# Kernel tuning notes

Hardware: AMD Instinct MI355X
Metric: run time of the kernel (lower is better)

## Reference

```python
import jax, jax.numpy as jnp
import numpy as np

B, S, D = 1, 2048, 4096
H, KVH, HD = 32, 8, 128


def setup_inputs() -> dict:
    key = jax.random.key(0)
    ks = jax.random.split(key, 6)
    x = jax.random.normal(ks[0], (B, S, D), dtype=jnp.float32)
    # Llama3 RoPE angles: theta = 500000
    inv_freq = 1.0 / (500000.0 ** (np.arange(0, HD, 2, dtype=np.float32) / HD))
    ang = np.arange(S, dtype=np.float32)[:, None] * inv_freq[None, :]  # [S, HD//2]
    freqs_cos = jnp.asarray(np.cos(ang), dtype=jnp.float32)
    freqs_sin = jnp.asarray(np.sin(ang), dtype=jnp.float32)
    sc = 0.02
    wq = jax.random.normal(ks[1], (H * HD, D), dtype=jnp.float32) * sc
    wk = jax.random.normal(ks[2], (KVH * HD, D), dtype=jnp.float32) * sc
    wv = jax.random.normal(ks[3], (KVH * HD, D), dtype=jnp.float32) * sc
    wo = jax.random.normal(ks[4], (D, H * HD), dtype=jnp.float32) * sc
    return {"x": x, "freqs_cos": freqs_cos, "freqs_sin": freqs_sin,
            "wq": wq, "wk": wk, "wv": wv, "wo": wo}


def _rope(t, cos, sin):
    # t: [B, S, h, HD]; rotate consecutive pairs (complex multiply)
    t2 = t.reshape(*t.shape[:-1], HD // 2, 2)
    x0, x1 = t2[..., 0], t2[..., 1]
    c = cos[None, :, None, :]
    s = sin[None, :, None, :]
    r0 = x0 * c - x1 * s
    r1 = x0 * s + x1 * c
    return jnp.stack([r0, r1], axis=-1).reshape(t.shape)


def reference(x, freqs_cos, freqs_sin, wq, wk, wv, wo):
    b, s, _ = x.shape
    q = jnp.einsum('bsd,ed->bse', x, wq).reshape(b, s, H, HD)
    k = jnp.einsum('bsd,ed->bse', x, wk).reshape(b, s, KVH, HD)
    v = jnp.einsum('bsd,ed->bse', x, wv).reshape(b, s, KVH, HD)
    q = _rope(q, freqs_cos, freqs_sin)
    k = _rope(k, freqs_cos, freqs_sin)
    # GQA: repeat kv heads
    rep = H // KVH
    k = jnp.repeat(k, rep, axis=2)
    v = jnp.repeat(v, rep, axis=2)
    scale = 1.0 / jnp.sqrt(jnp.asarray(HD, dtype=x.dtype))
    scores = jnp.einsum('bqhd,bkhd->bhqk', q, k) * scale
    causal = jnp.tril(jnp.ones((s, s), dtype=bool))
    scores = jnp.where(causal[None, None], scores, jnp.finfo(scores.dtype).min)
    p = jax.nn.softmax(scores, axis=-1)
    out = jnp.einsum('bhqk,bkhd->bqhd', p, v).reshape(b, s, H * HD)
    return jnp.einsum('bse,de->bsd', out, wo)
```

## Files before the change

kernel.cpp:

```cpp
#include <hip/hip_runtime.h>

typedef unsigned short u16;
typedef short bf16x8 __attribute__((ext_vector_type(8)));
typedef float f32x4 __attribute__((ext_vector_type(4)));

#define S_LEN 2048
#define ATT_SCALE (0.08838834764831845f * 1.4426950408889634f)
#define NEG_BIG  -1.0e30f

static __device__ __forceinline__ float bf2f(u16 u) {
  union { unsigned int i; float f; } v; v.i = ((unsigned int)u) << 16; return v.f;
}
static __device__ __forceinline__ u16 f2bf(float f) {
  union { float f; unsigned int i; } v; v.f = f;
  unsigned int x = v.i;
  return (u16)((x + 0x7fffu + ((x >> 16) & 1u)) >> 16);
}
static __device__ __forceinline__ float fexp2(float x) {
  return __builtin_amdgcn_exp2f(x);
}

static __device__ __forceinline__ void gl_lds16(const u16* g, u16* l) {
  __builtin_amdgcn_global_load_lds(
      (const __attribute__((address_space(1))) unsigned int*)g,
      (__attribute__((address_space(3))) unsigned int*)l, 16, 0, 0);
}

static __device__ __forceinline__ bf16x8 load8(const u16* p) { return *(const bf16x8*)p; }
static __device__ __forceinline__ bf16x8 load8(const float* p) {
  f32x4 a = *(const f32x4*)p;
  f32x4 b = *(const f32x4*)(p + 4);
  bf16x8 r;
  r[0] = (short)f2bf(a[0]); r[1] = (short)f2bf(a[1]);
  r[2] = (short)f2bf(a[2]); r[3] = (short)f2bf(a[3]);
  r[4] = (short)f2bf(b[0]); r[5] = (short)f2bf(b[1]);
  r[6] = (short)f2bf(b[2]); r[7] = (short)f2bf(b[3]);
  return r;
}
static __device__ __forceinline__ void store_out(u16* C, size_t i, float v)  { C[i] = f2bf(v); }
static __device__ __forceinline__ void store_out(float* C, size_t i, float v){ C[i] = v; }

__global__ __launch_bounds__(256) void f2b_kernel(
    const float* __restrict__ s, u16* __restrict__ d, int n8) {
  int i = blockIdx.x * 256 + threadIdx.x;
  if (i >= n8) return;
  *(bf16x8*)&d[(size_t)i * 8] = load8(s + (size_t)i * 8);
}

template <typename OT>
static __device__ __forceinline__ void gemm_core(
    const u16* __restrict__ A, const u16* __restrict__ B, OT* __restrict__ C,
    int K, int ldc, int bm, int bn) {
  __shared__ __align__(16) u16 As[128 * 64];
  __shared__ __align__(16) u16 Bs[128 * 64];
  const int tid  = threadIdx.x;
  const int lane = tid & 63;
  const int wave = tid >> 6;
  const int wm = (wave >> 1) << 6;
  const int wn = (wave & 1) << 6;
  const int col  = lane & 15;
  const int quad = lane >> 4;

  const f32x4 fzero = {0.f, 0.f, 0.f, 0.f};
  f32x4 acc[4][4];
#pragma unroll
  for (int i = 0; i < 4; ++i)
#pragma unroll
    for (int j = 0; j < 4; ++j) acc[i][j] = fzero;

  const int srow = (lane >> 3);
  const int sc8  = lane & 7;

  for (int k0 = 0; k0 < K; k0 += 64) {
#pragma unroll
    for (int i = 0; i < 4; ++i) {
      int r = wave * 32 + i * 8 + srow;
      int src = (sc8 ^ (r & 7)) << 3;
      gl_lds16(A + (size_t)(bm + r) * K + k0 + src, &As[(wave * 32 + i * 8) * 64]);
      gl_lds16(B + (size_t)(bn + r) * K + k0 + src, &Bs[(wave * 32 + i * 8) * 64]);
    }
    __syncthreads();
#pragma unroll
    for (int kk = 0; kk < 64; kk += 32) {
      bf16x8 af[4], bfr[4];
#pragma unroll
      for (int mt = 0; mt < 4; ++mt) {
        int row = wm + mt * 16 + col;
        af[mt] = *(const bf16x8*)&As[row * 64 + ((((kk >> 3) + quad) ^ (col & 7)) << 3)];
      }
#pragma unroll
      for (int nt = 0; nt < 4; ++nt) {
        int row = wn + nt * 16 + col;
        bfr[nt] = *(const bf16x8*)&Bs[row * 64 + ((((kk >> 3) + quad) ^ (col & 7)) << 3)];
      }
#pragma unroll
      for (int mt = 0; mt < 4; ++mt)
#pragma unroll
        for (int nt = 0; nt < 4; ++nt)
          acc[mt][nt] = __builtin_amdgcn_mfma_f32_16x16x32_bf16(
              af[mt], bfr[nt], acc[mt][nt], 0, 0, 0);
    }
    __syncthreads();
  }
#pragma unroll
  for (int mt = 0; mt < 4; ++mt)
#pragma unroll
    for (int nt = 0; nt < 4; ++nt)
#pragma unroll
      for (int r = 0; r < 4; ++r) {
        int row = bm + wm + mt * 16 + quad * 4 + r;
        int cn  = bn + wn + nt * 16 + col;
        store_out(C, (size_t)row * ldc + cn, acc[mt][nt][r]);
      }
}

__global__ __launch_bounds__(256) void gemm_qkv(
    const u16* __restrict__ xb, const u16* __restrict__ wqb,
    const u16* __restrict__ wkb, const u16* __restrict__ wvb,
    u16* __restrict__ q, u16* __restrict__ k, u16* __restrict__ v) {
  int bx = blockIdx.x;
  const u16* B; u16* C; int ldc, bn;
  if (bx < 32)      { B = wqb; C = q; ldc = 4096; bn = bx * 128; }
  else if (bx < 40) { B = wkb; C = k; ldc = 1024; bn = (bx - 32) * 128; }
  else              { B = wvb; C = v; ldc = 1024; bn = (bx - 40) * 128; }
  gemm_core<u16>(xb, B, C, 4096, ldc, blockIdx.y * 128, bn);
}

__global__ __launch_bounds__(256) void gemm_o(
    const u16* __restrict__ ao, const u16* __restrict__ wob, float* __restrict__ out) {
  gemm_core<float>(ao, wob, out, 4096, 4096, blockIdx.y * 128, blockIdx.x * 128);
}

#define LDK 72
template <typename AT, typename BT, typename OT>
__global__ __launch_bounds__(256) void gemm_bt(
    const AT* __restrict__ A, const BT* __restrict__ B,
    OT* __restrict__ C, int M, int N, int K) {
  __shared__ __align__(16) u16 As[128 * LDK];
  __shared__ __align__(16) u16 Bs[128 * LDK];
  const int tid  = threadIdx.x;
  const int lane = tid & 63;
  const int wave = tid >> 6;
  const int wm = (wave >> 1) << 6;
  const int wn = (wave & 1) << 6;
  const int col  = lane & 15;
  const int quad = lane >> 4;
  const int bm = blockIdx.y * 128;
  const int bn = blockIdx.x * 128;

  const f32x4 fzero = {0.f, 0.f, 0.f, 0.f};
  f32x4 acc[4][4];
#pragma unroll
  for (int i = 0; i < 4; ++i)
#pragma unroll
    for (int j = 0; j < 4; ++j) acc[i][j] = fzero;

  const int sr = tid >> 3;
  const int sc = (tid & 7) * 8;
  const AT* Aptr = A + (size_t)(bm + sr) * K + sc;
  const BT* Bptr = B + (size_t)(bn + sr) * K + sc;

  for (int k0 = 0; k0 < K; k0 += 64) {
#pragma unroll
    for (int p = 0; p < 4; ++p) {
      *(bf16x8*)&As[(sr + 32 * p) * LDK + sc] = load8(Aptr + (size_t)(32 * p) * K + k0);
      *(bf16x8*)&Bs[(sr + 32 * p) * LDK + sc] = load8(Bptr + (size_t)(32 * p) * K + k0);
    }
    __syncthreads();
#pragma unroll
    for (int kk = 0; kk < 64; kk += 32) {
      bf16x8 af[4], bfr[4];
#pragma unroll
      for (int mt = 0; mt < 4; ++mt)
        af[mt] = *(const bf16x8*)&As[(wm + mt * 16 + col) * LDK + kk + quad * 8];
#pragma unroll
      for (int nt = 0; nt < 4; ++nt)
        bfr[nt] = *(const bf16x8*)&Bs[(wn + nt * 16 + col) * LDK + kk + quad * 8];
#pragma unroll
      for (int mt = 0; mt < 4; ++mt)
#pragma unroll
        for (int nt = 0; nt < 4; ++nt)
          acc[mt][nt] = __builtin_amdgcn_mfma_f32_16x16x32_bf16(
              af[mt], bfr[nt], acc[mt][nt], 0, 0, 0);
    }
    __syncthreads();
  }
#pragma unroll
  for (int mt = 0; mt < 4; ++mt)
#pragma unroll
    for (int nt = 0; nt < 4; ++nt)
#pragma unroll
      for (int r = 0; r < 4; ++r) {
        int row = bm + wm + mt * 16 + quad * 4 + r;
        int cn  = bn + wn + nt * 16 + col;
        store_out(C, (size_t)row * N + cn, acc[mt][nt][r]);
      }
}

__global__ __launch_bounds__(256) void rope_kernel(
    u16* __restrict__ q, u16* __restrict__ k,
    const float* __restrict__ cs, const float* __restrict__ sn) {
  int idx = blockIdx.x * 256 + threadIdx.x;
  const int QP = S_LEN * 32 * 64;
  u16* base;
  int s, i;
  bool isq = idx < QP;
  if (isq) {
    s = idx >> 11; int w = idx & 2047; i = w & 63;
    base = q + (size_t)s * 4096 + (w >> 6) * 128 + 2 * i;
  } else {
    int j = idx - QP;
    s = j >> 9; int w = j & 511; i = w & 63;
    base = k + (size_t)s * 1024 + (w >> 6) * 128 + 2 * i;
  }
  float c  = cs[s * 64 + i];
  float sv = sn[s * 64 + i];
  float x0 = bf2f(base[0]);
  float x1 = bf2f(base[1]);
  float r0 = x0 * c - x1 * sv;
  float r1 = x0 * sv + x1 * c;
  if (isq) { r0 *= ATT_SCALE; r1 *= ATT_SCALE; }
  base[0] = f2bf(r0);
  base[1] = f2bf(r1);
}

__global__ __launch_bounds__(512, 2) void attn_kernel(
    const u16* __restrict__ Q, const u16* __restrict__ K,
    const u16* __restrict__ V, u16* __restrict__ O) {
  const int ib   = blockIdx.x;
  const int h    = blockIdx.y;
  const int kvh  = h >> 2;
  const int tid  = threadIdx.x;
  const int lane = tid & 63;
  const int wave = tid >> 6;
  const int grp  = wave >> 2;
  const int wl   = wave & 3;
  const int col  = lane & 15;
  const int quad = lane >> 4;
  const int chd  = col >> 3;
  const int gt   = tid & 255;

  __shared__ __align__(16) u16 SMEM[2][16384];
  __shared__ float MLS[256];
  u16* Kb = &SMEM[grp][0];
  u16* Vb = &SMEM[grp][8192];

  const f32x4 fzero = {0.f, 0.f, 0.f, 0.f};

  const int krow = lane >> 4;
  const int kcnk = lane & 15;
  const int vsc  = (gt & 15) * 8;
  const int vrp  = gt >> 4;
  const int vrot = gt & 7;

  for (int t = 0; t < 2; ++t) {
    const int qb = t ? 15 - ib : ib;
    const int rb = qb * 128 + wl * 32;

    bf16x8 qf[2][4];
#pragma unroll
    for (int u = 0; u < 2; ++u)
#pragma unroll
      for (int kb = 0; kb < 4; ++kb)
        qf[u][kb] = *(const bf16x8*)&Q[(size_t)(rb + u * 16 + col) * 4096 +
                                       h * 128 + kb * 32 + quad * 8];

    f32x4 oacc[2][8];
#pragma unroll
    for (int u = 0; u < 2; ++u)
#pragma unroll
      for (int nt = 0; nt < 8; ++nt) oacc[u][nt] = fzero;
    float m_[2] = {NEG_BIG, NEG_BIG};
    float l_[2] = {0.f, 0.f};

    const int nr = qb + 1;
    for (int rnd = 0; rnd < nr; ++rnd) {
      const int c    = grp * nr + rnd;
      const int pos0 = c * 64;

#pragma unroll
      for (int i = 0; i < 4; ++i) {
        int r  = wl * 16 + i * 4 + krow;
        int g  = (kcnk & 8) |
                 ((((kcnk ^ r) & 7) + (((r >> 3) & 1) << 2)) & 7);
        gl_lds16(&K[(size_t)(pos0 + r) * 1024 + kvh * 128 + g * 8],
                 &Kb[(wl * 16 + i * 4) * 128]);
      }
#pragma unroll
      for (int it = 0; it < 2; ++it) {
        int rp = vrp + it * 16;
        const u16* vp = &V[(size_t)(pos0 + 2 * rp) * 1024 + kvh * 128 + vsc];
        union { bf16x8 v; u16 u[8]; } ue, uo;
        ue.v = *(const bf16x8*)vp;
        uo.v = *(const bf16x8*)(vp + 1024);
        int pc = rp >> 2, pi = rp & 3;
#pragma unroll
        for (int j = 0; j < 8; ++j) {
          int jj = (j + vrot) & 7;
          int hd = vsc + jj;
          int swz = (((pc + (((hd >> 3) & 1) << 2)) & 7) ^ (hd & 7));
          unsigned val = (unsigned)ue.u[jj] | ((unsigned)uo.u[jj] << 16);
          *(unsigned*)&Vb[hd * 64 + swz * 8 + pi * 2] = val;
        }
      }
      __syncthreads();

      f32x4 sv[2][4];
#pragma unroll
      for (int u = 0; u < 2; ++u)
#pragma unroll
        for (int kv = 0; kv < 4; ++kv) sv[u][kv] = fzero;
      __builtin_amdgcn_s_setprio(1);
#pragma unroll
      for (int kv = 0; kv < 4; ++kv) {
        int r = kv * 16 + col;
#pragma unroll
        for (int kb = 0; kb < 4; ++kb) {
          int kq   = kb * 4 + quad;
          int slot = (kq & 8) | ((((kq & 7) + (chd << 2)) & 7) ^ (r & 7));
          bf16x8 kf = *(const bf16x8*)&Kb[r * 128 + slot * 8];
          sv[0][kv] = __builtin_amdgcn_mfma_f32_16x16x32_bf16(kf, qf[0][kv*0+kb], sv[0][kv], 0, 0, 0);
          sv[1][kv] = __builtin_amdgcn_mfma_f32_16x16x32_bf16(kf, qf[1][kb], sv[1][kv], 0, 0, 0);
        }
      }
      __builtin_amdgcn_s_setprio(0);

      unsigned pk[2][4][2];
#pragma unroll
      for (int u = 0; u < 2; ++u) {
        const int ubase = rb + u * 16;
        const int qpos  = ubase + col;
        const bool nomask = (pos0 + 63 <= ubase);
        float mx = NEG_BIG;
        if (nomask) {
#pragma unroll
          for (int kv = 0; kv < 4; ++kv)
#pragma unroll
            for (int r = 0; r < 4; ++r) mx = fmaxf(mx, sv[u][kv][r]);
        } else {
#pragma unroll
          for (int kv = 0; kv < 4; ++kv)
#pragma unroll
            for (int r = 0; r < 4; ++r) {
              bool keep = (pos0 + kv * 16 + quad * 4 + r) <= qpos;
              float s = keep ? sv[u][kv][r] : NEG_BIG;
              sv[u][kv][r] = s;
              mx = fmaxf(mx, s);
            }
        }
        mx = fmaxf(mx, __shfl_xor(mx, 16));
        mx = fmaxf(mx, __shfl_xor(mx, 32));
        if (!__all(mx - m_[u] <= 8.f)) {
          float mnew  = fmaxf(m_[u], mx);
          float alpha = fexp2(m_[u] - mnew);
          l_[u] *= alpha;
#pragma unroll
          for (int nt = 0; nt < 8; ++nt) {
            oacc[u][nt][0] *= alpha; oacc[u][nt][1] *= alpha;
            oacc[u][nt][2] *= alpha; oacc[u][nt][3] *= alpha;
          }
          m_[u] = mnew;
        }
        float ls = 0.f;
        if (nomask) {
#pragma unroll
          for (int kv = 0; kv < 4; ++kv)
#pragma unroll
            for (int r = 0; r < 4; ++r) {
              float p = fexp2(sv[u][kv][r] - m_[u]);
              sv[u][kv][r] = p;
              ls += p;
            }
        } else {
#pragma unroll
          for (int kv = 0; kv < 4; ++kv)
#pragma unroll
            for (int r = 0; r < 4; ++r) {
              float p = fexp2(sv[u][kv][r] - m_[u]);
              bool keep = (pos0 + kv * 16 + quad * 4 + r) <= qpos;
              p = keep ? p : 0.f;
              sv[u][kv][r] = p;
              ls += p;
            }
        }
        ls += __shfl_xor(ls, 16);
        ls += __shfl_xor(ls, 32);
        l_[u] += ls;
#pragma unroll
        for (int kv = 0; kv < 4; ++kv) {
          pk[u][kv][0] = (unsigned)f2bf(sv[u][kv][0]) | ((unsigned)f2bf(sv[u][kv][1]) << 16);
          pk[u][kv][1] = (unsigned)f2bf(sv[u][kv][2]) | ((unsigned)f2bf(sv[u][kv][3]) << 16);
        }
      }

      const int idxA = col + 16 * (2 * (quad & 1));
      const int idxB = idxA + 16;
      const bool hi  = quad >= 2;
#pragma unroll
      for (int kc = 0; kc < 2; ++kc) {
        union { unsigned u[4]; bf16x8 v; } pb[2];
#pragma unroll
        for (int u = 0; u < 2; ++u) {
          unsigned a00 = __shfl(pk[u][2 * kc][0],     idxA);
          unsigned a01 = __shfl(pk[u][2 * kc][1],     idxA);
          unsigned a10 = __shfl(pk[u][2 * kc + 1][0], idxA);
          unsigned a11 = __shfl(pk[u][2 * kc + 1][1], idxA);
          unsigned b00 = __shfl(pk[u][2 * kc][0],     idxB);
          unsigned b01 = __shfl(pk[u][2 * kc][1],     idxB);
          unsigned b10 = __shfl(pk[u][2 * kc + 1][0], idxB);
          unsigned b11 = __shfl(pk[u][2 * kc + 1][1], idxB);
          pb[u].u[0] = hi ? a10 : a00;
          pb[u].u[1] = hi ? a11 : a01;
          pb[u].u[2] = hi ? b10 : b00;
          pb[u].u[3] = hi ? b11 : b01;
        }
        __builtin_amdgcn_s_setprio(1);
#pragma unroll
        for (int nt = 0; nt < 8; ++nt) {
          int hd  = nt * 16 + col;
          int pc  = kc * 4 + quad;
          int swz = (((pc + (chd << 2)) & 7) ^ (hd & 7));
          bf16x8 vf = *(const bf16x8*)&Vb[hd * 64 + swz * 8];
          oacc[0][nt] = __builtin_amdgcn_mfma_f32_16x16x32_bf16(vf, pb[0].v, oacc[0][nt], 0, 0, 0);
          oacc[1][nt] = __builtin_amdgcn_mfma_f32_16x16x32_bf16(vf, pb[1].v, oacc[1][nt], 0, 0, 0);
        }
        __builtin_amdgcn_s_setprio(0);
      }
      __syncthreads();
    }

    float* MF = (float*)&SMEM[0][0];
    if (grp == 1) {
#pragma unroll
      for (int u = 0; u < 2; ++u) {
        int ql = wl * 32 + u * 16 + col;
#pragma unroll
        for (int nt = 0; nt < 8; ++nt)
          *(f32x4*)&MF[(size_t)ql * 128 + nt * 16 + quad * 4] = oacc[u][nt];
        if (quad == 0) { MLS[2 * ql] = m_[u]; MLS[2 * ql + 1] = l_[u]; }
      }
    }
    __syncthreads();
    if (grp == 0) {
#pragma unroll
      for (int u = 0; u < 2; ++u) {
        int ql = wl * 32 + u * 16 + col;
        int qpos = qb * 128 + ql;
        float m1 = MLS[2 * ql], l1 = MLS[2 * ql + 1];
        float mn = fmaxf(m_[u], m1);
        float a0 = fexp2(m_[u] - mn), a1 = fexp2(m1 - mn);
        float li = 1.f / (l_[u] * a0 + l1 * a1);
        a0 *= li; a1 *= li;
#pragma unroll
        for (int nt = 0; nt < 8; ++nt) {
          f32x4 o1 = *(const f32x4*)&MF[(size_t)ql * 128 + nt * 16 + quad * 4];
          union { u16 u[4]; unsigned long long ll; } w;
          w.u[0] = f2bf(oacc[u][nt][0] * a0 + o1[0] * a1);
          w.u[1] = f2bf(oacc[u][nt][1] * a0 + o1[1] * a1);
          w.u[2] = f2bf(oacc[u][nt][2] * a0 + o1[2] * a1);
          w.u[3] = f2bf(oacc[u][nt][3] * a0 + o1[3] * a1);
          *(unsigned long long*)&O[(size_t)qpos * 4096 + h * 128 + nt * 16 + quad * 4] = w.ll;
        }
      }
    }
    __syncthreads();
  }
}

extern "C" void kernel_launch(void* const* d_in, const int* in_sizes, int n_in,
                              void* d_out, int out_size, void* d_ws, size_t ws_size,
                              hipStream_t stream) {
  const float* x  = (const float*)d_in[0];
  const float* fc = (const float*)d_in[1];
  const float* fs = (const float*)d_in[2];
  const float* wq = (const float*)d_in[3];
  const float* wk = (const float*)d_in[4];
  const float* wv = (const float*)d_in[5];
  const float* wo = (const float*)d_in[6];
  float* out = (float*)d_out;

  u16* q  = (u16*)d_ws;
  u16* k  = q + (size_t)8388608;
  u16* v  = k + (size_t)2097152;
  u16* ao = v + (size_t)2097152;

  dim3 blk(256, 1, 1);
  dim3 ablk(512, 1, 1);
  const size_t NEED_FAST = 109051904ULL;

  if (ws_size >= NEED_FAST) {
    u16* xb  = ao  + (size_t)8388608;
    u16* wqb = xb  + (size_t)8388608;
    u16* wkb = wqb + (size_t)16777216;
    u16* wvb = wkb + (size_t)4194304;
    u16* wob = wqb;

    hipLaunchKernelGGL(f2b_kernel, dim3(4096, 1, 1), blk, 0, stream, x,  xb,  1048576);
    hipLaunchKernelGGL(f2b_kernel, dim3(8192, 1, 1), blk, 0, stream, wq, wqb, 2097152);
    hipLaunchKernelGGL(f2b_kernel, dim3(2048, 1, 1), blk, 0, stream, wk, wkb, 524288);
    hipLaunchKernelGGL(f2b_kernel, dim3(2048, 1, 1), blk, 0, stream, wv, wvb, 524288);
    hipLaunchKernelGGL(gemm_qkv, dim3(48, 16, 1), blk, 0, stream, xb, wqb, wkb, wvb, q, k, v);
    hipLaunchKernelGGL(f2b_kernel, dim3(8192, 1, 1), blk, 0, stream, wo, wob, 2097152);
    hipLaunchKernelGGL(rope_kernel, dim3(20480, 1, 1), blk, 0, stream, q, k, fc, fs);
    hipLaunchKernelGGL(attn_kernel, dim3(8, 32, 1), ablk, 0, stream, q, k, v, ao);
    hipLaunchKernelGGL(gemm_o, dim3(32, 16, 1), blk, 0, stream, ao, wob, out);
  } else {
    hipLaunchKernelGGL((gemm_bt<float, float, u16>), dim3(32, 16, 1), blk, 0, stream,
                       x, wq, q, 2048, 4096, 4096);
    hipLaunchKernelGGL((gemm_bt<float, float, u16>), dim3(8, 16, 1),  blk, 0, stream,
                       x, wk, k, 2048, 1024, 4096);
    hipLaunchKernelGGL((gemm_bt<float, float, u16>), dim3(8, 16, 1),  blk, 0, stream,
                       x, wv, v, 2048, 1024, 4096);
    hipLaunchKernelGGL(rope_kernel, dim3(20480, 1, 1), blk, 0, stream, q, k, fc, fs);
    hipLaunchKernelGGL(attn_kernel, dim3(8, 32, 1), ablk, 0, stream, q, k, v, ao);
    hipLaunchKernelGGL((gemm_bt<u16, float, float>), dim3(32, 16, 1), blk, 0, stream,
                       ao, wo, out, 2048, 4096, 4096);
  }
}
```

Baseline: 537.5 us.

## Load K fragments directly to registers with prefetch, remap attention blocks, fuse casts

The attention kernel no longer stages K through LDS. Each wave loads its K MFMA fragments straight from global memory into registers and prefetches the next chunk while softmax runs. The block index is remapped so that co-scheduled blocks share heads/KV data, and the merge buffer gets its own LDS array. The four fp32-to-bf16 conversion launches are fused into a single grid-stride kernel. Trade-offs: higher register pressure (64 extra VGPRs for kfr) under launch_bounds(512,2), redundant global K reads across waves, and larger LDS footprint.

```diff
diff --git a/kernel.cpp b/kernel.cpp
--- a/kernel.cpp
+++ b/kernel.cpp
@@ -39,6 +39,22 @@
 }
 static __device__ __forceinline__ void store_out(u16* C, size_t i, float v)  { C[i] = f2bf(v); }
 static __device__ __forceinline__ void store_out(float* C, size_t i, float v){ C[i] = v; }
+
+__global__ __launch_bounds__(256) void f2b4_kernel(
+    const float* __restrict__ x,  const float* __restrict__ wq,
+    const float* __restrict__ wk, const float* __restrict__ wv,
+    u16* __restrict__ xb, u16* __restrict__ wqb,
+    u16* __restrict__ wkb, u16* __restrict__ wvb) {
+  const int total = 4194304;
+  for (int u = blockIdx.x * 256 + threadIdx.x; u < total; u += gridDim.x * 256) {
+    const float* s; u16* d; int off;
+    if (u < 1048576)      { s = x;  d = xb;  off = u; }
+    else if (u < 3145728) { s = wq; d = wqb; off = u - 1048576; }
+    else if (u < 3670016) { s = wk; d = wkb; off = u - 3145728; }
+    else                  { s = wv; d = wvb; off = u - 3670016; }
+    *(bf16x8*)&d[(size_t)off * 8] = load8(s + (size_t)off * 8);
+  }
+}
 
 __global__ __launch_bounds__(256) void f2b_kernel(
     const float* __restrict__ s, u16* __restrict__ d, int n8) {
@@ -227,8 +243,10 @@
 __global__ __launch_bounds__(512, 2) void attn_kernel(
     const u16* __restrict__ Q, const u16* __restrict__ K,
     const u16* __restrict__ V, u16* __restrict__ O) {
-  const int ib   = blockIdx.x;
-  const int h    = blockIdx.y;
+  const int sw   = blockIdx.x + blockIdx.y * 8;
+  const int L    = (sw & 7) * 32 + (sw >> 3);
+  const int ib   = L & 7;
+  const int h    = L >> 3;
   const int kvh  = h >> 2;
   const int tid  = threadIdx.x;
   const int lane = tid & 63;
@@ -240,15 +258,13 @@
   const int chd  = col >> 3;
   const int gt   = tid & 255;
 
-  __shared__ __align__(16) u16 SMEM[2][16384];
+  __shared__ __align__(16) u16 VS[2][8192];
+  __shared__ __align__(16) float MF[128 * 128];
   __shared__ float MLS[256];
-  u16* Kb = &SMEM[grp][0];
-  u16* Vb = &SMEM[grp][8192];
+  u16* Vb = &VS[grp][0];
 
   const f32x4 fzero = {0.f, 0.f, 0.f, 0.f};
 
-  const int krow = lane >> 4;
-  const int kcnk = lane & 15;
   const int vsc  = (gt & 15) * 8;
   const int vrp  = gt >> 4;
   const int vrot = gt & 7;
@@ -274,18 +290,23 @@
     float l_[2] = {0.f, 0.f};
 
     const int nr = qb + 1;
+    const int c0 = grp * nr;
+
+    bf16x8 kfr[4][4];
+    {
+      const int p0 = c0 * 64;
+#pragma unroll
+      for (int kv = 0; kv < 4; ++kv)
+#pragma unroll
+        for (int kb = 0; kb < 4; ++kb)
+          kfr[kv][kb] = *(const bf16x8*)&K[(size_t)(p0 + kv * 16 + col) * 1024 +
+                                           kvh * 128 + kb * 32 + quad * 8];
+    }
+
     for (int rnd = 0; rnd < nr; ++rnd) {
-      const int c    = grp * nr + rnd;
+      const int c    = c0 + rnd;
       const int pos0 = c * 64;
 
-#pragma unroll
-      for (int i = 0; i < 4; ++i) {
-        int r  = wl * 16 + i * 4 + krow;
-        int g  = (kcnk & 8) |
-                 ((((kcnk ^ r) & 7) + (((r >> 3) & 1) << 2)) & 7);
-        gl_lds16(&K[(size_t)(pos0 + r) * 1024 + kvh * 128 + g * 8],
-                 &Kb[(wl * 16 + i * 4) * 128]);
-      }
 #pragma unroll
       for (int it = 0; it < 2; ++it) {
         int rp = vrp + it * 16;
@@ -312,18 +333,23 @@
         for (int kv = 0; kv < 4; ++kv) sv[u][kv] = fzero;
       __builtin_amdgcn_s_setprio(1);
 #pragma unroll
-      for (int kv = 0; kv < 4; ++kv) {
-        int r = kv * 16 + col;
+      for (int kv = 0; kv < 4; ++kv)
 #pragma unroll
         for (int kb = 0; kb < 4; ++kb) {
-          int kq   = kb * 4 + quad;
-          int slot = (kq & 8) | ((((kq & 7) + (chd << 2)) & 7) ^ (r & 7));
-          bf16x8 kf = *(const bf16x8*)&Kb[r * 128 + slot * 8];
-          sv[0][kv] = __builtin_amdgcn_mfma_f32_16x16x32_bf16(kf, qf[0][kv*0+kb], sv[0][kv], 0, 0, 0);
-          sv[1][kv] = __builtin_amdgcn_mfma_f32_16x16x32_bf16(kf, qf[1][kb], sv[1][kv], 0, 0, 0);
-        }
-      }
+          sv[0][kv] = __builtin_amdgcn_mfma_f32_16x16x32_bf16(kfr[kv][kb], qf[0][kb], sv[0][kv], 0, 0, 0);
+          sv[1][kv] = __builtin_amdgcn_mfma_f32_16x16x32_bf16(kfr[kv][kb], qf[1][kb], sv[1][kv], 0, 0, 0);
+        }
       __builtin_amdgcn_s_setprio(0);
+
+      if (rnd + 1 < nr) {
+        const int p1 = (c + 1) * 64;
+#pragma unroll
+        for (int kv = 0; kv < 4; ++kv)
+#pragma unroll
+          for (int kb = 0; kb < 4; ++kb)
+            kfr[kv][kb] = *(const bf16x8*)&K[(size_t)(p1 + kv * 16 + col) * 1024 +
+                                             kvh * 128 + kb * 32 + quad * 8];
+      }
 
       unsigned pk[2][4][2];
 #pragma unroll
@@ -429,7 +455,6 @@
       __syncthreads();
     }
 
-    float* MF = (float*)&SMEM[0][0];
     if (grp == 1) {
 #pragma unroll
       for (int u = 0; u < 2; ++u) {
@@ -495,11 +520,10 @@
     u16* wvb = wkb + (size_t)4194304;
     u16* wob = wqb;
 
-    hipLaunchKernelGGL(f2b_kernel, dim3(4096, 1, 1), blk, 0, stream, x,  xb,  1048576);
-    hipLaunchKernelGGL(f2b_kernel, dim3(8192, 1, 1), blk, 0, stream, wq, wqb, 2097152);
-    hipLaunchKernelGGL(f2b_kernel, dim3(2048, 1, 1), blk, 0, stream, wk, wkb, 524288);
-    hipLaunchKernelGGL(f2b_kernel, dim3(2048, 1, 1), blk, 0, stream, wv, wvb, 524288);
-    hipLaunchKernelGGL(gemm_qkv, dim3(48, 16, 1), blk, 0, stream, xb, wqb, wkb, wvb, q, k, v);
+    hipLaunchKernelGGL(f2b4_kernel, dim3(2048, 1, 1), blk, 0, stream,
+                       x, wq, wk, wv, xb, wqb, wkb, wvb);
+    hipLaunchKernelGGL(gemm_qkv, dim3(48, 16, 1), blk, 0, stream,
+                       xb, wqb, wkb, wvb, q, k, v);
     hipLaunchKernelGGL(f2b_kernel, dim3(8192, 1, 1), blk, 0, stream, wo, wob, 2097152);
     hipLaunchKernelGGL(rope_kernel, dim3(20480, 1, 1), blk, 0, stream, q, k, fc, fs);
     hipLaunchKernelGGL(attn_kernel, dim3(8, 32, 1), ablk, 0, stream, q, k, v, ao);
```

Result: slower. 612.2 us (+13.9%).
